# Optimization experiments

Measured on AMD Instinct MI355X. Metric: run time of the kernel, lower is better.

The kernel has to match this reference:

```python
import jax, jax.numpy as jnp
import numpy as np

H = 8
D = 64
EPS = 1e-5
TEMP = 1.0


def _ln(x, w, b):
    m = jnp.mean(x, axis=-1, keepdims=True)
    v = jnp.var(x, axis=-1, keepdims=True)
    return (x - m) * jax.lax.rsqrt(v + EPS) * w + b


def setup_inputs() -> dict:
    key = jax.random.key(0)
    ks = jax.random.split(key, 8)
    B, T, C = 4, 1024, 512
    x = jax.random.normal(ks[0], (B, T, C), dtype=jnp.float32)
    pair = jax.random.normal(ks[1], (B, T, T, H), dtype=jnp.float32)
    mask = jax.random.randint(ks[2], (B, T, T), 0, 2).astype(bool)
    s = 0.02
    return {
        "x": x,
        "pair": pair,
        "mask": mask,
        "norm_w": jnp.ones((C,), jnp.float32),
        "norm_b": jnp.zeros((C,), jnp.float32),
        "qkv_w": jax.random.normal(ks[3], (3 * C, C), jnp.float32) * s,
        "qkv_b": jnp.zeros((3 * C,), jnp.float32),
        "qln_w": jnp.ones((C,), jnp.float32),
        "qln_b": jnp.zeros((C,), jnp.float32),
        "kln_w": jnp.ones((C,), jnp.float32),
        "kln_b": jnp.zeros((C,), jnp.float32),
        "proj_w": jax.random.normal(ks[4], (C, C), jnp.float32) * s,
        "proj_b": jnp.zeros((C,), jnp.float32),
    }


def reference(x, pair, mask, norm_w, norm_b, qkv_w, qkv_b, qln_w, qln_b,
              kln_w, kln_b, proj_w, proj_b):
    B, T, C = x.shape
    # pre-norm
    xn = _ln(x, norm_w, norm_b)
    qkv = xn @ qkv_w.T + qkv_b  # [B,T,3C]
    q, k, v = jnp.split(qkv, 3, axis=-1)
    q = _ln(q, qln_w, qln_b)
    k = _ln(k, kln_w, kln_b)
    # [B,T,C] -> [B,H,T,D]
    to_heads = lambda t: t.reshape(B, T, H, D).transpose(0, 2, 1, 3)
    q, k, v = to_heads(q), to_heads(k), to_heads(v)
    scale = (D ** -0.5) / TEMP
    sim = jnp.einsum("bhid,bhjd->bhij", q, k) * scale
    sim = sim + pair.transpose(0, 3, 1, 2)  # additive pair bias [B,H,T,T]
    neg = jnp.finfo(sim.dtype).min
    sim = jnp.where(mask[:, None, :, :], sim, sim + neg)
    attn = jax.nn.softmax(sim, axis=-1)
    out = jnp.einsum("bhij,bhjd->bhid", attn, v)
    out = out.transpose(0, 2, 1, 3).reshape(B, T, C)
    return out @ proj_w.T + proj_b
```

## Files before the change

### kernel.cpp

```cpp
#include <hip/hip_runtime.h>
#include <math.h>

#define B_  4
#define T_  1024
#define C_  512
#define H_  8
#define D_  64
#define N3_ 1536
#define BT_ 4096

constexpr float kEps = 1e-5f;
constexpr float kNeg = -3.4028234663852886e38f;
constexpr float kMaskNeg = -1.4e38f;
constexpr float kLog2e = 1.44269504088896f;
constexpr float kShift2 = 17.312340490667562f;

typedef __attribute__((ext_vector_type(8))) short bf16x8;
typedef __attribute__((ext_vector_type(4))) float f32x4;

__device__ __forceinline__ short f2bf(float f) {
  union { float f; unsigned u; } v; v.f = f;
  unsigned r = v.u + 0x7FFFu + ((v.u >> 16) & 1u);
  return (short)(r >> 16);
}
__device__ __forceinline__ float bf2f(unsigned short b) {
  union { unsigned u; float f; } v;
  v.u = ((unsigned)b) << 16;
  return v.f;
}

__device__ __forceinline__ void gld16(const void* g, void* l) {
  __builtin_amdgcn_global_load_lds(
      (const __attribute__((address_space(1))) unsigned int*)g,
      (__attribute__((address_space(3))) unsigned int*)l, 16, 0, 0);
}

__global__ __launch_bounds__(64) void mask_detect_kernel(
    const unsigned int* __restrict__ m, int* __restrict__ flag) {
  int lane = threadIdx.x;
  int any_big = 0;
#pragma unroll
  for (int p = 0; p < 16; ++p) {
    unsigned int v = m[lane + p * 64];
    any_big |= (v > 1u);
  }
  unsigned long long b = __ballot(any_big);
  if (lane == 0) flag[0] = (b != 0ull) ? 1 : 0;
}

__global__ __launch_bounds__(256) void mask_convert_kernel(
    const void* __restrict__ mraw, const int* __restrict__ flag,
    uchar4* __restrict__ out) {
  int idx = blockIdx.x * 256 + threadIdx.x;
  uchar4 v;
  if (flag[0]) {
    v = ((const uchar4*)mraw)[idx];
    v.x = v.x ? 1 : 0; v.y = v.y ? 1 : 0; v.z = v.z ? 1 : 0; v.w = v.w ? 1 : 0;
  } else {
    int4 w = ((const int4*)mraw)[idx];
    v = make_uchar4(w.x != 0, w.y != 0, w.z != 0, w.w != 0);
  }
  out[idx] = v;
}

__global__ __launch_bounds__(256) void pair_prep_kernel(
    const float* __restrict__ pair, const void* __restrict__ mraw,
    short* __restrict__ biast) {
  __shared__ short P[8][1024 + 8];
  unsigned wv = ((const unsigned*)mraw)[threadIdx.x];
  int is_u8 = __syncthreads_or(wv > 1u);
  int bi = blockIdx.x;
  int b = bi >> 10, i = bi & 1023;
  int tid = threadIdx.x;
  const float* src = pair + (size_t)bi * (T_ * H_);
#pragma unroll
  for (int p = 0; p < 8; ++p) {
    int c = tid + p * 256;
    int j = c >> 1, hh = (c & 1) * 4;
    float4 v = *(const float4*)&src[c * 4];
    P[hh + 0][j] = f2bf(v.x * kLog2e);
    P[hh + 1][j] = f2bf(v.y * kLog2e);
    P[hh + 2][j] = f2bf(v.z * kLog2e);
    P[hh + 3][j] = f2bf(v.w * kLog2e);
  }
  bool mk[4];
  if (is_u8) {
    uchar4 mv = ((const uchar4*)mraw)[bi * 256 + tid];
    mk[0] = mv.x; mk[1] = mv.y; mk[2] = mv.z; mk[3] = mv.w;
  } else {
    int4 mv = ((const int4*)mraw)[bi * 256 + tid];
    mk[0] = mv.x != 0; mk[1] = mv.y != 0; mk[2] = mv.z != 0; mk[3] = mv.w != 0;
  }
  __syncthreads();
  const short negb = f2bf(kMaskNeg);
  int j = tid * 4;
#pragma unroll
  for (int h = 0; h < 8; ++h) {
    short4 o;
    o.x = mk[0] ? P[h][j + 0] : negb;
    o.y = mk[1] ? P[h][j + 1] : negb;
    o.z = mk[2] ? P[h][j + 2] : negb;
    o.w = mk[3] ? P[h][j + 3] : negb;
    *(short4*)&biast[((size_t)(b * 8 + h) * T_ + i) * T_ + j] = o;
  }
}

__global__ __launch_bounds__(256) void wcvt2_kernel(
    const float* __restrict__ a, short* __restrict__ oa,
    const float* __restrict__ b, short* __restrict__ ob, int nblk_a) {
  int bid = blockIdx.x;
  const float* src; short* dst; int idx;
  if (bid < nblk_a) { src = a; dst = oa; idx = bid * 256 + threadIdx.x; }
  else             { src = b; dst = ob; idx = (bid - nblk_a) * 256 + threadIdx.x; }
  int i = idx * 4;
  float4 v = *(const float4*)&src[i];
  short4 o;
  o.x = f2bf(v.x); o.y = f2bf(v.y); o.z = f2bf(v.z); o.w = f2bf(v.w);
  *(short4*)&dst[i] = o;
}

__global__ __launch_bounds__(128) void ln_x_kernel(
    const float* __restrict__ x, const float* __restrict__ w,
    const float* __restrict__ b, short* __restrict__ xn) {
  int row = blockIdx.x;
  int tid = threadIdx.x;
  const float* xr = x + (size_t)row * C_;
  float4 v = *(const float4*)&xr[tid * 4];
  float s  = v.x + v.y + v.z + v.w;
  float ss = v.x * v.x + v.y * v.y + v.z * v.z + v.w * v.w;
#pragma unroll
  for (int o = 32; o > 0; o >>= 1) {
    s  += __shfl_down(s, o);
    ss += __shfl_down(ss, o);
  }
  __shared__ float sh[4];
  int wid = tid >> 6, lane = tid & 63;
  if (lane == 0) { sh[wid] = s; sh[2 + wid] = ss; }
  __syncthreads();
  float m   = (sh[0] + sh[1]) * (1.0f / C_);
  float var = (sh[2] + sh[3]) * (1.0f / C_) - m * m;
  float inv = rsqrtf(var + kEps);
  float4 wv = *(const float4*)&w[tid * 4];
  float4 bv = *(const float4*)&b[tid * 4];
  short4 o4;
  o4.x = f2bf((v.x - m) * inv * wv.x + bv.x);
  o4.y = f2bf((v.y - m) * inv * wv.y + bv.y);
  o4.z = f2bf((v.z - m) * inv * wv.z + bv.z);
  o4.w = f2bf((v.w - m) * inv * wv.w + bv.w);
  *(short4*)&xn[(size_t)row * C_ + tid * 4] = o4;
}

__global__ __launch_bounds__(256) void gemm_bf16_128_kernel(
    const short* __restrict__ A, const short* __restrict__ W,
    const float* __restrict__ bias, float* __restrict__ Cmat,
    int M, int N, int K) {
  __shared__ short As[128 * 64];
  __shared__ short Bs[128 * 64];
  int tid = threadIdx.x;
  int lane = tid & 63, wave = tid >> 6;
  int wm = wave >> 1, wn = wave & 1;
  int col = lane & 15, quad = lane >> 4;
  int m0 = blockIdx.y * 128, n0 = blockIdx.x * 128;
  int wbase = tid & ~63;

  f32x4 acc[4][4];
#pragma unroll
  for (int mi = 0; mi < 4; ++mi)
#pragma unroll
    for (int ni = 0; ni < 4; ++ni) acc[mi][ni] = {0.f, 0.f, 0.f, 0.f};

  for (int k0 = 0; k0 < K; k0 += 64) {
    __syncthreads();
#pragma unroll
    for (int p = 0; p < 4; ++p) {
      int c = tid + p * 256;
      int row = c >> 3, kc = (c & 7) * 8;
      gld16(&A[(size_t)(m0 + row) * K + k0 + kc], &As[(wbase + p * 256) * 8]);
    }
#pragma unroll
    for (int p = 0; p < 4; ++p) {
      int c = tid + p * 256;
      int row = c >> 3, kc = (c & 7) * 8;
      gld16(&W[(size_t)(n0 + row) * K + k0 + kc], &Bs[(wbase + p * 256) * 8]);
    }
    __syncthreads();
#pragma unroll
    for (int s = 0; s < 2; ++s) {
      bf16x8 af[4], bfv[4];
#pragma unroll
      for (int mi = 0; mi < 4; ++mi)
        af[mi] = *(const bf16x8*)&As[(64 * wm + 16 * mi + col) * 64 + s * 32 + quad * 8];
#pragma unroll
      for (int ni = 0; ni < 4; ++ni)
        bfv[ni] = *(const bf16x8*)&Bs[(64 * wn + 16 * ni + col) * 64 + s * 32 + quad * 8];
#pragma unroll
      for (int mi = 0; mi < 4; ++mi)
#pragma unroll
        for (int ni = 0; ni < 4; ++ni)
          acc[mi][ni] = __builtin_amdgcn_mfma_f32_16x16x32_bf16(
              af[mi], bfv[ni], acc[mi][ni], 0, 0, 0);
    }
  }
#pragma unroll
  for (int ni = 0; ni < 4; ++ni) {
    int n = n0 + 64 * wn + 16 * ni + col;
    float bv = bias[n];
#pragma unroll
    for (int mi = 0; mi < 4; ++mi) {
#pragma unroll
      for (int r = 0; r < 4; ++r) {
        int m = m0 + 64 * wm + 16 * mi + quad * 4 + r;
        Cmat[(size_t)m * N + n] = acc[mi][ni][r] + bv;
      }
    }
  }
}

__global__ __launch_bounds__(256) void gemm_bf16_kernel(
    const short* __restrict__ A, const short* __restrict__ W,
    const float* __restrict__ bias, float* __restrict__ Cmat,
    int M, int N, int K) {
  __shared__ short As[128 * 64];
  __shared__ short Bs[64 * 64];
  int tid = threadIdx.x;
  int lane = tid & 63, wave = tid >> 6;
  int wm = wave >> 1, wn = wave & 1;
  int col = lane & 15, quad = lane >> 4;
  int m0 = blockIdx.y * 128, n0 = blockIdx.x * 64;
  int wbase = tid & ~63;

  f32x4 acc[4][2];
#pragma unroll
  for (int mi = 0; mi < 4; ++mi)
#pragma unroll
    for (int ni = 0; ni < 2; ++ni) acc[mi][ni] = {0.f, 0.f, 0.f, 0.f};

  for (int k0 = 0; k0 < K; k0 += 64) {
    __syncthreads();
#pragma unroll
    for (int p = 0; p < 4; ++p) {
      int c = tid + p * 256;
      int row = c >> 3, kc = (c & 7) * 8;
      gld16(&A[(size_t)(m0 + row) * K + k0 + kc], &As[(wbase + p * 256) * 8]);
    }
#pragma unroll
    for (int p = 0; p < 2; ++p) {
      int c = tid + p * 256;
      int row = c >> 3, kc = (c & 7) * 8;
      gld16(&W[(size_t)(n0 + row) * K + k0 + kc], &Bs[(wbase + p * 256) * 8]);
    }
    __syncthreads();
#pragma unroll
    for (int s = 0; s < 2; ++s) {
      bf16x8 af[4], bfv[2];
#pragma unroll
      for (int mi = 0; mi < 4; ++mi)
        af[mi] = *(const bf16x8*)&As[(64 * wm + 16 * mi + col) * 64 + s * 32 + quad * 8];
#pragma unroll
      for (int ni = 0; ni < 2; ++ni)
        bfv[ni] = *(const bf16x8*)&Bs[(32 * wn + 16 * ni + col) * 64 + s * 32 + quad * 8];
#pragma unroll
      for (int mi = 0; mi < 4; ++mi)
#pragma unroll
        for (int ni = 0; ni < 2; ++ni)
          acc[mi][ni] = __builtin_amdgcn_mfma_f32_16x16x32_bf16(
              af[mi], bfv[ni], acc[mi][ni], 0, 0, 0);
    }
  }
#pragma unroll
  for (int ni = 0; ni < 2; ++ni) {
    int n = n0 + 32 * wn + 16 * ni + col;
    float bv = bias[n];
#pragma unroll
    for (int mi = 0; mi < 4; ++mi) {
#pragma unroll
      for (int r = 0; r < 4; ++r) {
        int m = m0 + 64 * wm + 16 * mi + quad * 4 + r;
        Cmat[(size_t)m * N + n] = acc[mi][ni][r] + bv;
      }
    }
  }
}

__global__ __launch_bounds__(128) void qkv_ln_split_kernel(
    const float* __restrict__ qkv,
    const float* __restrict__ qw, const float* __restrict__ qb,
    const float* __restrict__ kw, const float* __restrict__ kb,
    short* __restrict__ qh, short* __restrict__ kh, short* __restrict__ vh) {
  int row = blockIdx.x;
  int b = row >> 10, t = row & 1023;
  int tid = threadIdx.x;
  const float* base = qkv + (size_t)row * N3_;
  int c4 = tid * 4;
  float4 qv = *(const float4*)&base[c4];
  float4 kv = *(const float4*)&base[C_ + c4];
  float4 vv = *(const float4*)&base[2 * C_ + c4];
  float sq  = qv.x + qv.y + qv.z + qv.w;
  float sqq = qv.x * qv.x + qv.y * qv.y + qv.z * qv.z + qv.w * qv.w;
  float sk  = kv.x + kv.y + kv.z + kv.w;
  float skk = kv.x * kv.x + kv.y * kv.y + kv.z * kv.z + kv.w * kv.w;
#pragma unroll
  for (int o = 32; o > 0; o >>= 1) {
    sq  += __shfl_down(sq, o);
    sqq += __shfl_down(sqq, o);
    sk  += __shfl_down(sk, o);
    skk += __shfl_down(skk, o);
  }
  __shared__ float sh[8];
  int wid = tid >> 6, lane = tid & 63;
  if (lane == 0) { sh[wid] = sq; sh[2 + wid] = sqq; sh[4 + wid] = sk; sh[6 + wid] = skk; }
  __syncthreads();
  float qm   = (sh[0] + sh[1]) * (1.0f / C_);
  float qvar = (sh[2] + sh[3]) * (1.0f / C_) - qm * qm;
  float km   = (sh[4] + sh[5]) * (1.0f / C_);
  float kvar = (sh[6] + sh[7]) * (1.0f / C_) - km * km;
  float qi = rsqrtf(qvar + kEps);
  float ki = rsqrtf(kvar + kEps);
  float4 qwv = *(const float4*)&qw[c4];
  float4 qbv = *(const float4*)&qb[c4];
  float4 kwv = *(const float4*)&kw[c4];
  float4 kbv = *(const float4*)&kb[c4];
  int h = tid >> 4;
  int d = (tid & 15) * 4;
  size_t dst = ((size_t)(b * H_ + h) * T_ + t) * D_ + d;
  short4 qo, ko, vo;
  qo.x = f2bf(((qv.x - qm) * qi * qwv.x + qbv.x) * 0.125f);
  qo.y = f2bf(((qv.y - qm) * qi * qwv.y + qbv.y) * 0.125f);
  qo.z = f2bf(((qv.z - qm) * qi * qwv.z + qbv.z) * 0.125f);
  qo.w = f2bf(((qv.w - qm) * qi * qwv.w + qbv.w) * 0.125f);
  ko.x = f2bf((kv.x - km) * ki * kwv.x + kbv.x);
  ko.y = f2bf((kv.y - km) * ki * kwv.y + kbv.y);
  ko.z = f2bf((kv.z - km) * ki * kwv.z + kbv.z);
  ko.w = f2bf((kv.w - km) * ki * kwv.w + kbv.w);
  vo.x = f2bf(vv.x); vo.y = f2bf(vv.y); vo.z = f2bf(vv.z); vo.w = f2bf(vv.w);
  *(short4*)&qh[dst] = qo;
  *(short4*)&kh[dst] = ko;
  *(short4*)&vh[dst] = vo;
}

__global__ __launch_bounds__(512, 4) void attn_split_kernel(
    const short* __restrict__ qh, const short* __restrict__ kh,
    const short* __restrict__ vh, const short* __restrict__ biast,
    float* __restrict__ Opart, float* __restrict__ lpart) {
  __shared__ short Ks[64 * 72];
  __shared__ short Vt[64 * 72];
  __shared__ short Ps[128 * 72];
  int tid = threadIdx.x;
  int lane = tid & 63, w = tid >> 6;
  int col = lane & 15, quad = lane >> 4;
  int bh = blockIdx.y;
  int half = blockIdx.z;
  int i0 = blockIdx.x * 128;
  const short* Qg = qh + (size_t)bh * T_ * D_;
  const short* Kg = kh + (size_t)bh * T_ * D_;
  const short* Vg = vh + (size_t)bh * T_ * D_;
  const unsigned short* Bpu =
      (const unsigned short*)(biast + (size_t)bh * T_ * T_);

  bf16x8 qf[2];
#pragma unroll
  for (int s = 0; s < 2; ++s)
    qf[s] = *(const bf16x8*)&Qg[(size_t)(i0 + 16 * w + col) * D_ + s * 32 + quad * 8];

  float lsum[4];
  f32x4 oacc[4];
#pragma unroll
  for (int r = 0; r < 4; ++r) lsum[r] = 0.f;
#pragma unroll
  for (int dt = 0; dt < 4; ++dt) oacc[dt] = {0.f, 0.f, 0.f, 0.f};

  int jbase = half * (T_ / 2);
  for (int jj = 0; jj < T_ / 2; jj += 64) {
    int j0 = jbase + jj;

    unsigned short bsv[4][4];
#pragma unroll
    for (int r = 0; r < 4; ++r) {
      int gi = i0 + 16 * w + quad * 4 + r;
#pragma unroll
      for (int jt = 0; jt < 4; ++jt)
        bsv[r][jt] = Bpu[(size_t)gi * T_ + j0 + 16 * jt + col];
    }

    __syncthreads();
    {
      int row = tid >> 3, dc = (tid & 7) * 8;
      *(int4*)&Ks[row * 72 + dc] =
          *(const int4*)&Kg[(size_t)(j0 + row) * D_ + dc];
    }
    {
      int j = tid & 63, d0 = (tid >> 6) * 8;
      short tmp[8];
      *(int4*)tmp = *(const int4*)&Vg[(size_t)(j0 + j) * D_ + d0];
#pragma unroll
      for (int q = 0; q < 8; ++q) Vt[(d0 + q) * 72 + j] = tmp[q];
    }
    __syncthreads();

    f32x4 sacc[4];
#pragma unroll
    for (int jt = 0; jt < 4; ++jt) sacc[jt] = {0.f, 0.f, 0.f, 0.f};
#pragma unroll
    for (int s = 0; s < 2; ++s) {
#pragma unroll
      for (int jt = 0; jt < 4; ++jt) {
        bf16x8 kf = *(const bf16x8*)&Ks[(16 * jt + col) * 72 + s * 32 + quad * 8];
        sacc[jt] = __builtin_amdgcn_mfma_f32_16x16x32_bf16(qf[s], kf, sacc[jt], 0, 0, 0);
      }
    }

#pragma unroll
    for (int r = 0; r < 4; ++r) {
      int li = 16 * w + quad * 4 + r;
#pragma unroll
      for (int jt = 0; jt < 4; ++jt) {
        float sv = fmaf(sacc[jt][r], kLog2e, bf2f(bsv[r][jt]));
        float p = exp2f(fminf(sv - kShift2, 86.5f));
        lsum[r] += p;
        Ps[li * 72 + 16 * jt + col] = f2bf(p);
      }
    }

#pragma unroll
    for (int s = 0; s < 2; ++s) {
      bf16x8 pf = *(const bf16x8*)&Ps[(16 * w + col) * 72 + s * 32 + quad * 8];
#pragma unroll
      for (int dt = 0; dt < 4; ++dt) {
        bf16x8 vf = *(const bf16x8*)&Vt[(16 * dt + col) * 72 + s * 32 + quad * 8];
        oacc[dt] = __builtin_amdgcn_mfma_f32_16x16x32_bf16(pf, vf, oacc[dt], 0, 0, 0);
      }
    }
  }

#pragma unroll
  for (int r = 0; r < 4; ++r) {
    float l = lsum[r];
#pragma unroll
    for (int o = 1; o < 16; o <<= 1) l += __shfl_xor(l, o);
    int gi = i0 + 16 * w + quad * 4 + r;
    size_t orow = (size_t)half * 32768 + (size_t)bh * T_ + gi;
    if (col == 0) lpart[orow] = l;
#pragma unroll
    for (int dt = 0; dt < 4; ++dt)
      Opart[orow * 64 + 16 * dt + col] = oacc[dt][r];
  }
}

__global__ __launch_bounds__(256) void attn_merge_kernel(
    const float* __restrict__ Opart, const float* __restrict__ lpart,
    short* __restrict__ ao) {
  int g = blockIdx.x * 256 + threadIdx.x;
  int row = g >> 4, d4 = (g & 15) * 4;
  float4 o0 = *(const float4*)&Opart[(size_t)row * 64 + d4];
  float4 o1 = *(const float4*)&Opart[((size_t)32768 + row) * 64 + d4];
  float inv = 1.0f / (lpart[row] + lpart[32768 + row]);
  int bh = row >> 10, gi = row & 1023;
  int b = bh >> 3, h = bh & 7;
  short4 o;
  o.x = f2bf((o0.x + o1.x) * inv);
  o.y = f2bf((o0.y + o1.y) * inv);
  o.z = f2bf((o0.z + o1.z) * inv);
  o.w = f2bf((o0.w + o1.w) * inv);
  *(short4*)&ao[((size_t)(b * T_ + gi)) * C_ + h * D_ + d4] = o;
}

__global__ __launch_bounds__(256) void attn_kernel(
    const short* __restrict__ qh, const short* __restrict__ kh,
    const short* __restrict__ vh, const float* __restrict__ pair,
    const unsigned char* __restrict__ mask, short* __restrict__ ao) {
  __shared__ short Ks[64 * 72];
  __shared__ short Vt[64 * 72];
  __shared__ short Ps[64 * 72];
  int tid = threadIdx.x;
  int lane = tid & 63, w = tid >> 6;
  int col = lane & 15, quad = lane >> 4;
  int bh = blockIdx.y;
  int b = bh >> 3, h = bh & 7;
  int i0 = blockIdx.x * 64;
  const short* Qg = qh + (size_t)bh * T_ * D_;
  const short* Kg = kh + (size_t)bh * T_ * D_;
  const short* Vg = vh + (size_t)bh * T_ * D_;

  bf16x8 qf[2];
#pragma unroll
  for (int s = 0; s < 2; ++s)
    qf[s] = *(const bf16x8*)&Qg[(size_t)(i0 + 16 * w + col) * D_ + s * 32 + quad * 8];

  float mrun[4], lrun[4];
  f32x4 oacc[4];
#pragma unroll
  for (int r = 0; r < 4; ++r) { mrun[r] = -INFINITY; lrun[r] = 0.f; }
#pragma unroll
  for (int dt = 0; dt < 4; ++dt) oacc[dt] = {0.f, 0.f, 0.f, 0.f};

  for (int j0 = 0; j0 < T_; j0 += 64) {
    __syncthreads();
#pragma unroll
    for (int p = 0; p < 2; ++p) {
      int c = tid + p * 256;
      int row = c >> 3, dc = (c & 7) * 8;
      *(int4*)&Ks[row * 72 + dc] =
          *(const int4*)&Kg[(size_t)(j0 + row) * D_ + dc];
    }
    {
      int j = tid & 63, d0 = (tid >> 6) * 16;
#pragma unroll
      for (int p = 0; p < 2; ++p) {
        short tmp[8];
        *(int4*)tmp = *(const int4*)&Vg[(size_t)(j0 + j) * D_ + d0 + p * 8];
#pragma unroll
        for (int q = 0; q < 8; ++q) Vt[(d0 + p * 8 + q) * 72 + j] = tmp[q];
      }
    }
    __syncthreads();

    f32x4 sacc[4];
#pragma unroll
    for (int jt = 0; jt < 4; ++jt) sacc[jt] = {0.f, 0.f, 0.f, 0.f};
#pragma unroll
    for (int s = 0; s < 2; ++s) {
#pragma unroll
      for (int jt = 0; jt < 4; ++jt) {
        bf16x8 kf = *(const bf16x8*)&Ks[(16 * jt + col) * 72 + s * 32 + quad * 8];
        sacc[jt] = __builtin_amdgcn_mfma_f32_16x16x32_bf16(qf[s], kf, sacc[jt], 0, 0, 0);
      }
    }

#pragma unroll
    for (int r = 0; r < 4; ++r) {
      int gi = i0 + 16 * w + quad * 4 + r;
      const float* prow = pair + (size_t)(b * T_ + gi) * (T_ * H_) + h;
      const unsigned char* mrow = mask + (size_t)(b * T_ + gi) * T_;
      float sv[4];
      float rm = -INFINITY;
#pragma unroll
      for (int jt = 0; jt < 4; ++jt) {
        int j = j0 + 16 * jt + col;
        float s = sacc[jt][r] + prow[(size_t)j * H_];
        if (!mrow[j]) s += kNeg;
        sv[jt] = s;
        rm = fmaxf(rm, s);
      }
#pragma unroll
      for (int o = 8; o > 0; o >>= 1) rm = fmaxf(rm, __shfl_xor(rm, o));
      float mnew  = fmaxf(mrun[r], rm);
      float alpha = __expf(mrun[r] - mnew);
      float psum = 0.f;
#pragma unroll
      for (int jt = 0; jt < 4; ++jt) {
        float p = __expf(sv[jt] - mnew);
        psum += p;
        Ps[(16 * w + quad * 4 + r) * 72 + 16 * jt + col] = f2bf(p);
      }
#pragma unroll
      for (int o = 8; o > 0; o >>= 1) psum += __shfl_xor(psum, o);
      lrun[r] = lrun[r] * alpha + psum;
      mrun[r] = mnew;
#pragma unroll
      for (int dt = 0; dt < 4; ++dt) oacc[dt][r] *= alpha;
    }
    __syncthreads();

#pragma unroll
    for (int s = 0; s < 2; ++s) {
      bf16x8 pf = *(const bf16x8*)&Ps[(16 * w + col) * 72 + s * 32 + quad * 8];
#pragma unroll
      for (int dt = 0; dt < 4; ++dt) {
        bf16x8 vf = *(const bf16x8*)&Vt[(16 * dt + col) * 72 + s * 32 + quad * 8];
        oacc[dt] = __builtin_amdgcn_mfma_f32_16x16x32_bf16(pf, vf, oacc[dt], 0, 0, 0);
      }
    }
  }

#pragma unroll
  for (int r = 0; r < 4; ++r) {
    int gi = i0 + 16 * w + quad * 4 + r;
    float inv = 1.0f / lrun[r];
    size_t base = (size_t)(b * T_ + gi) * C_ + h * D_;
#pragma unroll
    for (int dt = 0; dt < 4; ++dt)
      ao[base + 16 * dt + col] = f2bf(oacc[dt][r] * inv);
  }
}

extern "C" void kernel_launch(void* const* d_in, const int* in_sizes, int n_in,
                              void* d_out, int out_size, void* d_ws, size_t ws_size,
                              hipStream_t stream) {
  const float* x      = (const float*)d_in[0];
  const float* pair   = (const float*)d_in[1];
  const void*  maskraw = d_in[2];
  const float* norm_w = (const float*)d_in[3];
  const float* norm_b = (const float*)d_in[4];
  const float* qkv_w  = (const float*)d_in[5];
  const float* qkv_b  = (const float*)d_in[6];
  const float* qln_w  = (const float*)d_in[7];
  const float* qln_b  = (const float*)d_in[8];
  const float* kln_w  = (const float*)d_in[9];
  const float* kln_b  = (const float*)d_in[10];
  const float* proj_w = (const float*)d_in[11];
  const float* proj_b = (const float*)d_in[12];
  float* out = (float*)d_out;

  short* xn = (short*)d_out;
  short* qh = (short*)d_out + (size_t)BT_ * C_;

  const size_t MB = 1024 * 1024;

  if (ws_size >= 96 * MB) {
    char* base = (char*)d_ws;
    short* biast = (short*)base;
    float* qkv   = (float*)base;
    float* Opart = (float*)(base + 64 * MB);
    float* lpart = (float*)(base + 80 * MB);
    short* ao    = (short*)(base + 81 * MB);
    short* kh    = (short*)(base + 85 * MB);
    short* vh    = (short*)(base + 89 * MB);
    short* wq    = (short*)(base + 93 * MB);
    short* wp    = (short*)(base + 94 * MB + 512 * 1024);

    wcvt2_kernel<<<(N3_ * C_ + C_ * C_) / 1024, 256, 0, stream>>>(
        qkv_w, wq, proj_w, wp, (N3_ * C_) / 1024);
    ln_x_kernel<<<BT_, 128, 0, stream>>>(x, norm_w, norm_b, xn);
    gemm_bf16_128_kernel<<<dim3(N3_ / 128, BT_ / 128), 256, 0, stream>>>(
        xn, wq, qkv_b, qkv, BT_, N3_, C_);
    qkv_ln_split_kernel<<<BT_, 128, 0, stream>>>(
        qkv, qln_w, qln_b, kln_w, kln_b, qh, kh, vh);
    pair_prep_kernel<<<B_ * T_, 256, 0, stream>>>(pair, maskraw, biast);
    attn_split_kernel<<<dim3(T_ / 128, B_ * H_, 2), 512, 0, stream>>>(
        qh, kh, vh, biast, Opart, lpart);
    attn_merge_kernel<<<2048, 256, 0, stream>>>(Opart, lpart, ao);
    gemm_bf16_kernel<<<dim3(C_ / 64, BT_ / 128), 256, 0, stream>>>(
        ao, wp, proj_b, out, BT_, C_, C_);
  } else {
    float* qkv = (float*)d_ws;
    short* ao  = (short*)d_ws;
    short* sw  = (short*)d_ws;
    short* wq  = sw + (size_t)12 * 1024 * 1024;
    short* wp  = wq + (size_t)N3_ * C_;
    short* kh  = sw + (size_t)13 * 1024 * 1024;
    short* vh  = sw + (size_t)15 * 1024 * 1024;
    unsigned char* maskc = (unsigned char*)d_ws + (size_t)34 * MB;
    int* flag = (int*)((unsigned char*)d_ws + (size_t)38 * MB);

    mask_detect_kernel<<<1, 64, 0, stream>>>((const unsigned int*)maskraw, flag);
    mask_convert_kernel<<<(B_ * T_ * T_) / 1024, 256, 0, stream>>>(
        maskraw, flag, (uchar4*)maskc);
    wcvt2_kernel<<<(N3_ * C_ + C_ * C_) / 1024, 256, 0, stream>>>(
        qkv_w, wq, proj_w, wp, (N3_ * C_) / 1024);
    ln_x_kernel<<<BT_, 128, 0, stream>>>(x, norm_w, norm_b, xn);
    gemm_bf16_128_kernel<<<dim3(N3_ / 128, BT_ / 128), 256, 0, stream>>>(
        xn, wq, qkv_b, qkv, BT_, N3_, C_);
    qkv_ln_split_kernel<<<BT_, 128, 0, stream>>>(
        qkv, qln_w, qln_b, kln_w, kln_b, qh, kh, vh);
    attn_kernel<<<dim3(T_ / 64, B_ * H_), 256, 0, stream>>>(
        qh, kh, vh, pair, maskc, ao);
    gemm_bf16_kernel<<<dim3(C_ / 64, BT_ / 128), 256, 0, stream>>>(
        ao, wp, proj_b, out, BT_, C_, C_);
  }
}
```

Before: 316.0 us.

## Fuse QKV GEMM and pair-bias prep into one heterogeneous launch

The QKV projection GEMM (now 128x64 tiles) and the pair/mask bias preparation are merged into a single launch, with block index choosing the role, so the memory-bound pair conversion can overlap the compute-bound GEMM. Workspace layout is reshuffled so qkv no longer aliases the bias buffer, with kh placed in the output buffer. The bias-register loads in the attention loop move after the K/V shared-memory staging. The risks are a larger shared-memory footprint per block limiting occupancy, and the aliasing of kh and xn in d_out, which relies on stream ordering to be safe.

```diff
diff --git a/kernel.cpp b/kernel.cpp
--- a/kernel.cpp
+++ b/kernel.cpp
@@ -61,48 +61,6 @@
     v = make_uchar4(w.x != 0, w.y != 0, w.z != 0, w.w != 0);
   }
   out[idx] = v;
-}
-
-__global__ __launch_bounds__(256) void pair_prep_kernel(
-    const float* __restrict__ pair, const void* __restrict__ mraw,
-    short* __restrict__ biast) {
-  __shared__ short P[8][1024 + 8];
-  unsigned wv = ((const unsigned*)mraw)[threadIdx.x];
-  int is_u8 = __syncthreads_or(wv > 1u);
-  int bi = blockIdx.x;
-  int b = bi >> 10, i = bi & 1023;
-  int tid = threadIdx.x;
-  const float* src = pair + (size_t)bi * (T_ * H_);
-#pragma unroll
-  for (int p = 0; p < 8; ++p) {
-    int c = tid + p * 256;
-    int j = c >> 1, hh = (c & 1) * 4;
-    float4 v = *(const float4*)&src[c * 4];
-    P[hh + 0][j] = f2bf(v.x * kLog2e);
-    P[hh + 1][j] = f2bf(v.y * kLog2e);
-    P[hh + 2][j] = f2bf(v.z * kLog2e);
-    P[hh + 3][j] = f2bf(v.w * kLog2e);
-  }
-  bool mk[4];
-  if (is_u8) {
-    uchar4 mv = ((const uchar4*)mraw)[bi * 256 + tid];
-    mk[0] = mv.x; mk[1] = mv.y; mk[2] = mv.z; mk[3] = mv.w;
-  } else {
-    int4 mv = ((const int4*)mraw)[bi * 256 + tid];
-    mk[0] = mv.x != 0; mk[1] = mv.y != 0; mk[2] = mv.z != 0; mk[3] = mv.w != 0;
-  }
-  __syncthreads();
-  const short negb = f2bf(kMaskNeg);
-  int j = tid * 4;
-#pragma unroll
-  for (int h = 0; h < 8; ++h) {
-    short4 o;
-    o.x = mk[0] ? P[h][j + 0] : negb;
-    o.y = mk[1] ? P[h][j + 1] : negb;
-    o.z = mk[2] ? P[h][j + 2] : negb;
-    o.w = mk[3] ? P[h][j + 3] : negb;
-    *(short4*)&biast[((size_t)(b * 8 + h) * T_ + i) * T_ + j] = o;
-  }
 }
 
 __global__ __launch_bounds__(256) void wcvt2_kernel(
@@ -150,72 +108,6 @@
   *(short4*)&xn[(size_t)row * C_ + tid * 4] = o4;
 }
 
-__global__ __launch_bounds__(256) void gemm_bf16_128_kernel(
-    const short* __restrict__ A, const short* __restrict__ W,
-    const float* __restrict__ bias, float* __restrict__ Cmat,
-    int M, int N, int K) {
-  __shared__ short As[128 * 64];
-  __shared__ short Bs[128 * 64];
-  int tid = threadIdx.x;
-  int lane = tid & 63, wave = tid >> 6;
-  int wm = wave >> 1, wn = wave & 1;
-  int col = lane & 15, quad = lane >> 4;
-  int m0 = blockIdx.y * 128, n0 = blockIdx.x * 128;
-  int wbase = tid & ~63;
-
-  f32x4 acc[4][4];
-#pragma unroll
-  for (int mi = 0; mi < 4; ++mi)
-#pragma unroll
-    for (int ni = 0; ni < 4; ++ni) acc[mi][ni] = {0.f, 0.f, 0.f, 0.f};
-
-  for (int k0 = 0; k0 < K; k0 += 64) {
-    __syncthreads();
-#pragma unroll
-    for (int p = 0; p < 4; ++p) {
-      int c = tid + p * 256;
-      int row = c >> 3, kc = (c & 7) * 8;
-      gld16(&A[(size_t)(m0 + row) * K + k0 + kc], &As[(wbase + p * 256) * 8]);
-    }
-#pragma unroll
-    for (int p = 0; p < 4; ++p) {
-      int c = tid + p * 256;
-      int row = c >> 3, kc = (c & 7) * 8;
-      gld16(&W[(size_t)(n0 + row) * K + k0 + kc], &Bs[(wbase + p * 256) * 8]);
-    }
-    __syncthreads();
-#pragma unroll
-    for (int s = 0; s < 2; ++s) {
-      bf16x8 af[4], bfv[4];
-#pragma unroll
-      for (int mi = 0; mi < 4; ++mi)
-        af[mi] = *(const bf16x8*)&As[(64 * wm + 16 * mi + col) * 64 + s * 32 + quad * 8];
-#pragma unroll
-      for (int ni = 0; ni < 4; ++ni)
-        bfv[ni] = *(const bf16x8*)&Bs[(64 * wn + 16 * ni + col) * 64 + s * 32 + quad * 8];
-#pragma unroll
-      for (int mi = 0; mi < 4; ++mi)
-#pragma unroll
-        for (int ni = 0; ni < 4; ++ni)
-          acc[mi][ni] = __builtin_amdgcn_mfma_f32_16x16x32_bf16(
-              af[mi], bfv[ni], acc[mi][ni], 0, 0, 0);
-    }
-  }
-#pragma unroll
-  for (int ni = 0; ni < 4; ++ni) {
-    int n = n0 + 64 * wn + 16 * ni + col;
-    float bv = bias[n];
-#pragma unroll
-    for (int mi = 0; mi < 4; ++mi) {
-#pragma unroll
-      for (int r = 0; r < 4; ++r) {
-        int m = m0 + 64 * wm + 16 * mi + quad * 4 + r;
-        Cmat[(size_t)m * N + n] = acc[mi][ni][r] + bv;
-      }
-    }
-  }
-}
-
 __global__ __launch_bounds__(256) void gemm_bf16_kernel(
     const short* __restrict__ A, const short* __restrict__ W,
     const float* __restrict__ bias, float* __restrict__ Cmat,
@@ -278,6 +170,116 @@
         int m = m0 + 64 * wm + 16 * mi + quad * 4 + r;
         Cmat[(size_t)m * N + n] = acc[mi][ni][r] + bv;
       }
+    }
+  }
+}
+
+__global__ __launch_bounds__(256) void fused_pg_kernel(
+    const short* __restrict__ A, const short* __restrict__ W,
+    const float* __restrict__ bias, float* __restrict__ Cmat,
+    const float* __restrict__ pair, const void* __restrict__ mraw,
+    short* __restrict__ biast) {
+  __shared__ short smem[128 * 64 + 64 * 64];
+  int tid = threadIdx.x;
+  if (blockIdx.x < 768) {
+    short* As = smem;
+    short* Bs = smem + 128 * 64;
+    const int K = C_, N = N3_;
+    int lane = tid & 63;
+    int wave = tid >> 6;
+    int wm = wave >> 1, wn = wave & 1;
+    int col = lane & 15, quad = lane >> 4;
+    int g = blockIdx.x;
+    int n0 = (g % 24) * 64, m0 = (g / 24) * 128;
+    int wbase = tid & ~63;
+
+    f32x4 acc[4][2];
+#pragma unroll
+    for (int mi = 0; mi < 4; ++mi)
+#pragma unroll
+      for (int ni = 0; ni < 2; ++ni) acc[mi][ni] = {0.f, 0.f, 0.f, 0.f};
+
+    for (int k0 = 0; k0 < K; k0 += 64) {
+      __syncthreads();
+#pragma unroll
+      for (int p = 0; p < 4; ++p) {
+        int c = tid + p * 256;
+        int row = c >> 3, kc = (c & 7) * 8;
+        gld16(&A[(size_t)(m0 + row) * K + k0 + kc], &As[(wbase + p * 256) * 8]);
+      }
+#pragma unroll
+      for (int p = 0; p < 2; ++p) {
+        int c = tid + p * 256;
+        int row = c >> 3, kc = (c & 7) * 8;
+        gld16(&W[(size_t)(n0 + row) * K + k0 + kc], &Bs[(wbase + p * 256) * 8]);
+      }
+      __syncthreads();
+#pragma unroll
+      for (int s = 0; s < 2; ++s) {
+        bf16x8 af[4], bfv[2];
+#pragma unroll
+        for (int mi = 0; mi < 4; ++mi)
+          af[mi] = *(const bf16x8*)&As[(64 * wm + 16 * mi + col) * 64 + s * 32 + quad * 8];
+#pragma unroll
+        for (int ni = 0; ni < 2; ++ni)
+          bfv[ni] = *(const bf16x8*)&Bs[(32 * wn + 16 * ni + col) * 64 + s * 32 + quad * 8];
+#pragma unroll
+        for (int mi = 0; mi < 4; ++mi)
+#pragma unroll
+          for (int ni = 0; ni < 2; ++ni)
+            acc[mi][ni] = __builtin_amdgcn_mfma_f32_16x16x32_bf16(
+                af[mi], bfv[ni], acc[mi][ni], 0, 0, 0);
+      }
+    }
+#pragma unroll
+    for (int ni = 0; ni < 2; ++ni) {
+      int n = n0 + 32 * wn + 16 * ni + col;
+      float bv = bias[n];
+#pragma unroll
+      for (int mi = 0; mi < 4; ++mi) {
+#pragma unroll
+        for (int r = 0; r < 4; ++r) {
+          int m = m0 + 64 * wm + 16 * mi + quad * 4 + r;
+          Cmat[(size_t)m * N + n] = acc[mi][ni][r] + bv;
+        }
+      }
+    }
+  } else {
+    short (*P)[1032] = (short(*)[1032])smem;
+    unsigned wv = ((const unsigned*)mraw)[tid];
+    int is_u8 = __syncthreads_or(wv > 1u);
+    int bi = blockIdx.x - 768;
+    int b = bi >> 10, i = bi & 1023;
+    const float* src = pair + (size_t)bi * (T_ * H_);
+#pragma unroll
+    for (int p = 0; p < 8; ++p) {
+      int c = tid + p * 256;
+      int j = c >> 1, hh = (c & 1) * 4;
+      float4 v = *(const float4*)&src[c * 4];
+      P[hh + 0][j] = f2bf(v.x * kLog2e);
+      P[hh + 1][j] = f2bf(v.y * kLog2e);
+      P[hh + 2][j] = f2bf(v.z * kLog2e);
+      P[hh + 3][j] = f2bf(v.w * kLog2e);
+    }
+    bool mk[4];
+    if (is_u8) {
+      uchar4 mv = ((const uchar4*)mraw)[bi * 256 + tid];
+      mk[0] = mv.x; mk[1] = mv.y; mk[2] = mv.z; mk[3] = mv.w;
+    } else {
+      int4 mv = ((const int4*)mraw)[bi * 256 + tid];
+      mk[0] = mv.x != 0; mk[1] = mv.y != 0; mk[2] = mv.z != 0; mk[3] = mv.w != 0;
+    }
+    __syncthreads();
+    const short negb = f2bf(kMaskNeg);
+    int j = tid * 4;
+#pragma unroll
+    for (int h = 0; h < 8; ++h) {
+      short4 o;
+      o.x = mk[0] ? P[h][j + 0] : negb;
+      o.y = mk[1] ? P[h][j + 1] : negb;
+      o.z = mk[2] ? P[h][j + 2] : negb;
+      o.w = mk[3] ? P[h][j + 3] : negb;
+      *(short4*)&biast[((size_t)(b * 8 + h) * T_ + i) * T_ + j] = o;
     }
   }
 }
@@ -372,16 +374,6 @@
   int jbase = half * (T_ / 2);
   for (int jj = 0; jj < T_ / 2; jj += 64) {
     int j0 = jbase + jj;
-
-    unsigned short bsv[4][4];
-#pragma unroll
-    for (int r = 0; r < 4; ++r) {
-      int gi = i0 + 16 * w + quad * 4 + r;
-#pragma unroll
-      for (int jt = 0; jt < 4; ++jt)
-        bsv[r][jt] = Bpu[(size_t)gi * T_ + j0 + 16 * jt + col];
-    }
-
     __syncthreads();
     {
       int row = tid >> 3, dc = (tid & 7) * 8;
@@ -396,6 +388,15 @@
       for (int q = 0; q < 8; ++q) Vt[(d0 + q) * 72 + j] = tmp[q];
     }
     __syncthreads();
+
+    unsigned short bsv[4][4];
+#pragma unroll
+    for (int r = 0; r < 4; ++r) {
+      int gi = i0 + 16 * w + quad * 4 + r;
+#pragma unroll
+      for (int jt = 0; jt < 4; ++jt)
+        bsv[r][jt] = Bpu[(size_t)gi * T_ + j0 + 16 * jt + col];
+    }
 
     f32x4 sacc[4];
 #pragma unroll
@@ -601,37 +602,37 @@
   const float* proj_b = (const float*)d_in[12];
   float* out = (float*)d_out;
 
-  short* xn = (short*)d_out;
-  short* qh = (short*)d_out + (size_t)BT_ * C_;
-
   const size_t MB = 1024 * 1024;
 
   if (ws_size >= 96 * MB) {
     char* base = (char*)d_ws;
     short* biast = (short*)base;
-    float* qkv   = (float*)base;
+    float* qkv   = (float*)(base + 64 * MB);
     float* Opart = (float*)(base + 64 * MB);
     float* lpart = (float*)(base + 80 * MB);
     short* ao    = (short*)(base + 81 * MB);
-    short* kh    = (short*)(base + 85 * MB);
-    short* vh    = (short*)(base + 89 * MB);
-    short* wq    = (short*)(base + 93 * MB);
-    short* wp    = (short*)(base + 94 * MB + 512 * 1024);
+    short* vh    = (short*)(base + 88 * MB);
+    short* wq    = (short*)(base + 92 * MB);
+    short* wp    = (short*)(base + 93 * MB + 512 * 1024);
+    short* xn = (short*)d_out;
+    short* kh = (short*)d_out;
+    short* qh = (short*)d_out + (size_t)BT_ * C_;
 
     wcvt2_kernel<<<(N3_ * C_ + C_ * C_) / 1024, 256, 0, stream>>>(
         qkv_w, wq, proj_w, wp, (N3_ * C_) / 1024);
     ln_x_kernel<<<BT_, 128, 0, stream>>>(x, norm_w, norm_b, xn);
-    gemm_bf16_128_kernel<<<dim3(N3_ / 128, BT_ / 128), 256, 0, stream>>>(
-        xn, wq, qkv_b, qkv, BT_, N3_, C_);
+    fused_pg_kernel<<<768 + B_ * T_, 256, 0, stream>>>(
+        xn, wq, qkv_b, qkv, pair, maskraw, biast);
     qkv_ln_split_kernel<<<BT_, 128, 0, stream>>>(
         qkv, qln_w, qln_b, kln_w, kln_b, qh, kh, vh);
-    pair_prep_kernel<<<B_ * T_, 256, 0, stream>>>(pair, maskraw, biast);
     attn_split_kernel<<<dim3(T_ / 128, B_ * H_, 2), 512, 0, stream>>>(
         qh, kh, vh, biast, Opart, lpart);
     attn_merge_kernel<<<2048, 256, 0, stream>>>(Opart, lpart, ao);
     gemm_bf16_kernel<<<dim3(C_ / 64, BT_ / 128), 256, 0, stream>>>(
         ao, wp, proj_b, out, BT_, C_, C_);
   } else {
+    short* xn = (short*)d_out;
+    short* qh = (short*)d_out + (size_t)BT_ * C_;
     float* qkv = (float*)d_ws;
     short* ao  = (short*)d_ws;
     short* sw  = (short*)d_ws;
@@ -648,7 +649,7 @@
     wcvt2_kernel<<<(N3_ * C_ + C_ * C_) / 1024, 256, 0, stream>>>(
         qkv_w, wq, proj_w, wp, (N3_ * C_) / 1024);
     ln_x_kernel<<<BT_, 128, 0, stream>>>(x, norm_w, norm_b, xn);
-    gemm_bf16_128_kernel<<<dim3(N3_ / 128, BT_ / 128), 256, 0, stream>>>(
+    gemm_bf16_kernel<<<dim3(N3_ / 64, BT_ / 128), 256, 0, stream>>>(
         xn, wq, qkv_b, qkv, BT_, N3_, C_);
     qkv_ln_split_kernel<<<BT_, 128, 0, stream>>>(
         qkv, qln_w, qln_b, kln_w, kln_b, qh, kh, vh);
```

After: 318.0 us. About the same (+0.6%).
